# Kernel tuning notes

Hardware: AMD Instinct MI355X
Metric: run time of the kernel (lower is better)

The kernel has to match this reference:

```python
import jax, jax.numpy as jnp
import numpy as np


def _relative_position_index(ws):
    # matches SpatialAttention.build with qWh=qWw=kWh=kWw=ws
    coords = np.stack(np.meshgrid(np.arange(ws), np.arange(ws), indexing='ij'))
    cf = coords.reshape(2, -1)  # [2, N]
    rel = (cf[:, :, None] - cf[:, None, :]).transpose(1, 2, 0)  # [N, N, 2]
    rel[:, :, 0] += ws - 1
    rel[:, :, 1] += ws - 1
    rel[:, :, 0] *= 2 * ws - 1
    return rel.sum(-1)  # [N, N] int in [0, (2*ws-1)^2)


def _shift_mask(H, W, ws, ss):
    # standard Swin shifted-window attention mask: [num_windows, N, N]
    img = np.zeros((H, W))
    cnt = 0
    for h in (slice(0, -ws), slice(-ws, -ss), slice(-ss, None)):
        for w in (slice(0, -ws), slice(-ws, -ss), slice(-ss, None)):
            img[h, w] = cnt
            cnt += 1
    win = img.reshape(H // ws, ws, W // ws, ws).transpose(0, 2, 1, 3).reshape(-1, ws * ws)
    diff = win[:, None, :] - win[:, :, None]
    return np.where(diff != 0, -100.0, 0.0).astype(np.float32)


def _window_partition(x, ws):
    B, H, W, C = x.shape
    x = x.reshape(B, H // ws, ws, W // ws, ws, C)
    x = x.transpose(0, 1, 3, 2, 4, 5)
    return x.reshape(-1, ws, ws, C)  # [B*nW, ws, ws, C]


def _window_reverse(x, ws, H, W):
    C = x.shape[-1]
    x = x.reshape(-1, H // ws, W // ws, ws, ws, C)
    x = x.transpose(0, 1, 3, 2, 4, 5)
    return x.reshape(-1, H, W, C)


def setup_inputs() -> dict:
    key = jax.random.key(0)
    k1, k2, k3, k4 = jax.random.split(key, 4)
    B, H, W, C = 16, 64, 64, 512
    num_heads, ws = 16, 8
    return {
        'q': jax.random.normal(k1, (B, H, W, C), dtype=jnp.float32),
        'k': jax.random.normal(k2, (B, H, W, C), dtype=jnp.float32),
        'v': jax.random.normal(k3, (B, H, W, C), dtype=jnp.float32),
        'bias_table': jax.random.normal(k4, ((2 * ws - 1) ** 2, num_heads), dtype=jnp.float32) * 0.02,
        'num_heads': num_heads,
        'window_size': ws,
        'shift_size': 4,
    }


def reference(q, k, v, bias_table, num_heads, window_size, shift_size):
    B, H, W, C = q.shape
    ws, ss = window_size, shift_size
    N = ws * ws
    hd = C // num_heads
    scale = hd ** -0.5

    # cyclic shift
    q = jnp.roll(q, (-ss, -ss), axis=(1, 2))
    k = jnp.roll(k, (-ss, -ss), axis=(1, 2))
    v = jnp.roll(v, (-ss, -ss), axis=(1, 2))

    # window partition -> [B*nW, heads, N, hd]
    def to_heads(x):
        x = _window_partition(x, ws).reshape(-1, N, num_heads, hd)
        return x.transpose(0, 2, 1, 3)

    qh, kh, vh = to_heads(q), to_heads(k), to_heads(v)

    attn = jnp.einsum('bhid,bhjd->bhij', qh * scale, kh)  # [BnW, h, N, N]

    # gathered relative position bias: [1, h, N, N]
    idx = jnp.asarray(_relative_position_index(ws))
    rel_bias = bias_table[idx.reshape(-1)].reshape(N, N, num_heads).transpose(2, 0, 1)
    attn = attn + rel_bias[None]

    # shifted-window mask: [nW, N, N]
    mask = jnp.asarray(_shift_mask(H, W, ws, ss))
    nW = mask.shape[0]
    attn = attn.reshape(-1, nW, num_heads, N, N) + mask[None, :, None]
    attn = attn.reshape(-1, num_heads, N, N)

    attn = jax.nn.softmax(attn, axis=-1)

    x = jnp.einsum('bhij,bhjd->bihd', attn, vh).reshape(-1, ws, ws, C)
    x = _window_reverse(x, ws, H, W)
    x = jnp.roll(x, (ss, ss), axis=(1, 2))  # reverse cyclic shift
    return x
```

## Files before the change

### kernel.cpp

```cpp
#include <hip/hip_runtime.h>

#define TB 16
#define NHEADS 16
#define HD 32
#define WS 8
#define SS 4

typedef __attribute__((ext_vector_type(8))) __bf16 bf16x8;
typedef __attribute__((ext_vector_type(4))) float f32x4;

__device__ __forceinline__ unsigned short f2bf(float f) {
    unsigned u = __float_as_uint(f);
    u += 0x7fff + ((u >> 16) & 1);
    return (unsigned short)(u >> 16);
}
__device__ __forceinline__ unsigned pk2(float a, float b) {
    return (unsigned)f2bf(a) | ((unsigned)f2bf(b) << 16);
}
__device__ __forceinline__ float bf2f(unsigned short h) {
    return __uint_as_float(((unsigned)h) << 16);
}

#define OFF_Q 0
#define OFF_K 5120
#define OFF_P 0
#define OFF_V 10240
#define OFF_S 14848
#define OFF_B 23552

__global__ __launch_bounds__(64, 2)
void swin_attn_mfma(const float* __restrict__ q,
                    const float* __restrict__ k,
                    const float* __restrict__ v,
                    const float* __restrict__ bias_table,
                    float* __restrict__ out)
{
    __shared__ __align__(16) char smem[24464];
    char* sQ = smem + OFF_Q;
    char* sK = smem + OFF_K;
    char* sP = smem + OFF_P;
    char* sV = smem + OFF_V;
    char* sS = smem + OFF_S;
    float* sB = (float*)(smem + OFF_B);

    const int blk  = blockIdx.x;
    const int head = blk & (NHEADS - 1);
    const int win  = (blk >> 4) & 63;
    const int b    = blk >> 10;
    const int wh   = win >> 3;
    const int ww   = win & 7;

    const int lane = threadIdx.x;
    const int ih = lane >> 3, iw = lane & 7;
    const int quad = lane >> 4, lm = lane & 15;

    for (int t = lane; t < 225; t += 64)
        sB[t] = bias_table[t * NHEADS + head];

    const int gh = (wh * WS + ih + SS) & 63;
    const int gw = (ww * WS + iw + SS) & 63;
    const size_t rowbase = (((size_t)b * 64 + gh) * 64 + gw) * 512 + (size_t)head * HD;

    {
        const float scale = 0.17677669529663687f;
        const float4* qrow = (const float4*)(q + rowbase);
        uint4* qd = (uint4*)(sQ + lane * 80);
        #pragma unroll
        for (int t = 0; t < 4; ++t) {
            float4 a = qrow[2 * t], c = qrow[2 * t + 1];
            uint4 w;
            w.x = pk2(a.x * scale, a.y * scale);
            w.y = pk2(a.z * scale, a.w * scale);
            w.z = pk2(c.x * scale, c.y * scale);
            w.w = pk2(c.z * scale, c.w * scale);
            qd[t] = w;
        }
        const float4* krow = (const float4*)(k + rowbase);
        uint4* kd = (uint4*)(sK + lane * 80);
        #pragma unroll
        for (int t = 0; t < 4; ++t) {
            float4 a = krow[2 * t], c = krow[2 * t + 1];
            uint4 w;
            w.x = pk2(a.x, a.y);
            w.y = pk2(a.z, a.w);
            w.z = pk2(c.x, c.y);
            w.w = pk2(c.z, c.w);
            kd[t] = w;
        }
        const float4* vrow = (const float4*)(v + rowbase);
        #pragma unroll
        for (int t = 0; t < 8; ++t) {
            float4 x = vrow[t];
            *(unsigned short*)(sV + (4 * t + 0) * 144 + lane * 2) = f2bf(x.x);
            *(unsigned short*)(sV + (4 * t + 1) * 144 + lane * 2) = f2bf(x.y);
            *(unsigned short*)(sV + (4 * t + 2) * 144 + lane * 2) = f2bf(x.z);
            *(unsigned short*)(sV + (4 * t + 3) * 144 + lane * 2) = f2bf(x.w);
        }
    }
    __syncthreads();

    bf16x8 qa[4], kb[4];
    #pragma unroll
    for (int mt = 0; mt < 4; ++mt)
        qa[mt] = *(const bf16x8*)(sQ + (16 * mt + lm) * 80 + quad * 16);
    #pragma unroll
    for (int nt = 0; nt < 4; ++nt)
        kb[nt] = *(const bf16x8*)(sK + (16 * nt + lm) * 80 + quad * 16);

    f32x4 Sacc[4][4];
    #pragma unroll
    for (int mt = 0; mt < 4; ++mt)
        #pragma unroll
        for (int nt = 0; nt < 4; ++nt) {
            f32x4 z = {0.f, 0.f, 0.f, 0.f};
            Sacc[mt][nt] = __builtin_amdgcn_mfma_f32_16x16x32_bf16(qa[mt], kb[nt], z, 0, 0, 0);
        }

    #pragma unroll
    for (int mt = 0; mt < 4; ++mt)
        #pragma unroll
        for (int nt = 0; nt < 4; ++nt) {
            f32x4 s4 = Sacc[mt][nt];
            uint2 w;
            w.x = pk2(s4[0], s4[1]);
            w.y = pk2(s4[2], s4[3]);
            *(uint2*)(sS + (16 * nt + lm) * 136 + (16 * mt + 4 * quad) * 2) = w;
        }
    __syncthreads();

    float p[64];
    float l = 0.f;
    const bool eh = (wh == 7), ew = (ww == 7);
    const bool aH = (ih < 4), aW = (iw < 4);
    const char* bb = (const char*)sB + 4 * (ih * 15 + iw);
    const char* sc = sS + lane * 2;
    #pragma unroll
    for (int j = 0; j < 64; ++j) {
        const int jh = j >> 3, jw = j & 7;
        float s = bf2f(*(const unsigned short*)(sc + j * 136));
        s += *(const float*)(bb + 4 * ((7 - jh) * 15 + (7 - jw)));
        bool ok = (!eh || (aH == (jh < 4))) && (!ew || (aW == (jw < 4)));
        float e = ok ? __expf(s) : 0.f;
        p[j] = e;
        l += e;
    }
    const float rl = 1.f / l;
    {
        uint4* pd = (uint4*)(sP + lane * 144);
        #pragma unroll
        for (int t = 0; t < 8; ++t) {
            uint4 w;
            w.x = pk2(p[8 * t + 0] * rl, p[8 * t + 1] * rl);
            w.y = pk2(p[8 * t + 2] * rl, p[8 * t + 3] * rl);
            w.z = pk2(p[8 * t + 4] * rl, p[8 * t + 5] * rl);
            w.w = pk2(p[8 * t + 6] * rl, p[8 * t + 7] * rl);
            pd[t] = w;
        }
    }
    __syncthreads();

    bf16x8 pa[4][2], vb[2][2];
    #pragma unroll
    for (int mt = 0; mt < 4; ++mt)
        #pragma unroll
        for (int ks = 0; ks < 2; ++ks)
            pa[mt][ks] = *(const bf16x8*)(sP + (16 * mt + lm) * 144 + ks * 64 + quad * 16);
    #pragma unroll
    for (int nt = 0; nt < 2; ++nt)
        #pragma unroll
        for (int ks = 0; ks < 2; ++ks)
            vb[nt][ks] = *(const bf16x8*)(sV + (16 * nt + lm) * 144 + ks * 64 + quad * 16);

    f32x4 O[4][2];
    #pragma unroll
    for (int mt = 0; mt < 4; ++mt)
        #pragma unroll
        for (int nt = 0; nt < 2; ++nt) {
            f32x4 z = {0.f, 0.f, 0.f, 0.f};
            z = __builtin_amdgcn_mfma_f32_16x16x32_bf16(pa[mt][0], vb[nt][0], z, 0, 0, 0);
            O[mt][nt] = __builtin_amdgcn_mfma_f32_16x16x32_bf16(pa[mt][1], vb[nt][1], z, 0, 0, 0);
        }

    #pragma unroll
    for (int mt = 0; mt < 4; ++mt)
        #pragma unroll
        for (int r = 0; r < 4; ++r) {
            const int i = 16 * mt + 4 * quad + r;
            const int ghh = (wh * WS + (i >> 3) + SS) & 63;
            const int gww = (ww * WS + (i & 7) + SS) & 63;
            float* rp = out + (((size_t)b * 64 + ghh) * 64 + gww) * 512 + (size_t)head * HD + lm;
            rp[0]  = O[mt][0][r];
            rp[16] = O[mt][1][r];
        }
}

extern "C" void kernel_launch(void* const* d_in, const int* in_sizes, int n_in,
                              void* d_out, int out_size, void* d_ws, size_t ws_size,
                              hipStream_t stream) {
    const float* q  = (const float*)d_in[0];
    const float* k  = (const float*)d_in[1];
    const float* v  = (const float*)d_in[2];
    const float* bt = (const float*)d_in[3];
    float* out = (float*)d_out;

    dim3 grid(TB * 64 * NHEADS);
    dim3 block(64);
    swin_attn_mfma<<<grid, block, 0, stream>>>(q, k, v, bt, out);
}
```

Baseline: 438.9 us.

## Split window attention across four waves with in-register softmax

Each block now uses 256 threads (four waves). Wave 0 loads Q, wave 1 loads K, and waves 2 and 3 split V and the bias gather, so the global loads run in parallel. Each wave then computes one 16-row M tile of QK^T and applies bias, mask and exp directly on the MFMA accumulator registers. Row sums come from cross-lane shuffles, which removes the bf16 score round-trip through shared memory and the 64-element per-thread softmax loop. This lowers per-thread register and LDS pressure at the cost of an extra barrier and scattered 2-byte LDS stores for P.

```diff
diff --git a/kernel.cpp b/kernel.cpp
--- a/kernel.cpp
+++ b/kernel.cpp
@@ -17,30 +17,25 @@
 __device__ __forceinline__ unsigned pk2(float a, float b) {
     return (unsigned)f2bf(a) | ((unsigned)f2bf(b) << 16);
 }
-__device__ __forceinline__ float bf2f(unsigned short h) {
-    return __uint_as_float(((unsigned)h) << 16);
-}
 
 #define OFF_Q 0
 #define OFF_K 5120
 #define OFF_P 0
 #define OFF_V 10240
-#define OFF_S 14848
-#define OFF_B 23552
+#define OFF_B 14848
 
-__global__ __launch_bounds__(64, 2)
+__global__ __launch_bounds__(256, 8)
 void swin_attn_mfma(const float* __restrict__ q,
                     const float* __restrict__ k,
                     const float* __restrict__ v,
                     const float* __restrict__ bias_table,
                     float* __restrict__ out)
 {
-    __shared__ __align__(16) char smem[24464];
+    __shared__ __align__(16) char smem[15760];
     char* sQ = smem + OFF_Q;
     char* sK = smem + OFF_K;
     char* sP = smem + OFF_P;
     char* sV = smem + OFF_V;
-    char* sS = smem + OFF_S;
     float* sB = (float*)(smem + OFF_B);
 
     const int blk  = blockIdx.x;
@@ -50,148 +45,141 @@
     const int wh   = win >> 3;
     const int ww   = win & 7;
 
-    const int lane = threadIdx.x;
-    const int ih = lane >> 3, iw = lane & 7;
+    const int tid  = threadIdx.x;
+    const int wave = tid >> 6;
+    const int lane = tid & 63;
     const int quad = lane >> 4, lm = lane & 15;
 
-    for (int t = lane; t < 225; t += 64)
-        sB[t] = bias_table[t * NHEADS + head];
+    {
+        const int ih = lane >> 3, iw = lane & 7;
+        const int gh = (wh * WS + ih + SS) & 63;
+        const int gw = (ww * WS + iw + SS) & 63;
+        const size_t rowbase = (((size_t)b * 64 + gh) * 64 + gw) * 512 + (size_t)head * HD;
 
-    const int gh = (wh * WS + ih + SS) & 63;
-    const int gw = (ww * WS + iw + SS) & 63;
-    const size_t rowbase = (((size_t)b * 64 + gh) * 64 + gw) * 512 + (size_t)head * HD;
-
-    {
-        const float scale = 0.17677669529663687f;
-        const float4* qrow = (const float4*)(q + rowbase);
-        uint4* qd = (uint4*)(sQ + lane * 80);
-        #pragma unroll
-        for (int t = 0; t < 4; ++t) {
-            float4 a = qrow[2 * t], c = qrow[2 * t + 1];
-            uint4 w;
-            w.x = pk2(a.x * scale, a.y * scale);
-            w.y = pk2(a.z * scale, a.w * scale);
-            w.z = pk2(c.x * scale, c.y * scale);
-            w.w = pk2(c.z * scale, c.w * scale);
-            qd[t] = w;
-        }
-        const float4* krow = (const float4*)(k + rowbase);
-        uint4* kd = (uint4*)(sK + lane * 80);
-        #pragma unroll
-        for (int t = 0; t < 4; ++t) {
-            float4 a = krow[2 * t], c = krow[2 * t + 1];
-            uint4 w;
-            w.x = pk2(a.x, a.y);
-            w.y = pk2(a.z, a.w);
-            w.z = pk2(c.x, c.y);
-            w.w = pk2(c.z, c.w);
-            kd[t] = w;
-        }
-        const float4* vrow = (const float4*)(v + rowbase);
-        #pragma unroll
-        for (int t = 0; t < 8; ++t) {
-            float4 x = vrow[t];
-            *(unsigned short*)(sV + (4 * t + 0) * 144 + lane * 2) = f2bf(x.x);
-            *(unsigned short*)(sV + (4 * t + 1) * 144 + lane * 2) = f2bf(x.y);
-            *(unsigned short*)(sV + (4 * t + 2) * 144 + lane * 2) = f2bf(x.z);
-            *(unsigned short*)(sV + (4 * t + 3) * 144 + lane * 2) = f2bf(x.w);
+        if (wave == 0) {
+            const float scale = 0.17677669529663687f;
+            const float4* qrow = (const float4*)(q + rowbase);
+            uint4* qd = (uint4*)(sQ + lane * 80);
+            #pragma unroll
+            for (int t = 0; t < 4; ++t) {
+                float4 a = qrow[2 * t], c = qrow[2 * t + 1];
+                uint4 w;
+                w.x = pk2(a.x * scale, a.y * scale);
+                w.y = pk2(a.z * scale, a.w * scale);
+                w.z = pk2(c.x * scale, c.y * scale);
+                w.w = pk2(c.z * scale, c.w * scale);
+                qd[t] = w;
+            }
+        } else if (wave == 1) {
+            const float4* krow = (const float4*)(k + rowbase);
+            uint4* kd = (uint4*)(sK + lane * 80);
+            #pragma unroll
+            for (int t = 0; t < 4; ++t) {
+                float4 a = krow[2 * t], c = krow[2 * t + 1];
+                uint4 w;
+                w.x = pk2(a.x, a.y);
+                w.y = pk2(a.z, a.w);
+                w.z = pk2(c.x, c.y);
+                w.w = pk2(c.z, c.w);
+                kd[t] = w;
+            }
+        } else {
+            const int t0 = (wave == 2) ? 0 : 4;
+            const float4* vrow = (const float4*)(v + rowbase);
+            #pragma unroll
+            for (int t = 0; t < 4; ++t) {
+                float4 x = vrow[t0 + t];
+                const int ch = 4 * (t0 + t);
+                *(unsigned short*)(sV + (ch + 0) * 144 + lane * 2) = f2bf(x.x);
+                *(unsigned short*)(sV + (ch + 1) * 144 + lane * 2) = f2bf(x.y);
+                *(unsigned short*)(sV + (ch + 2) * 144 + lane * 2) = f2bf(x.z);
+                *(unsigned short*)(sV + (ch + 3) * 144 + lane * 2) = f2bf(x.w);
+            }
+            if (wave == 3) {
+                #pragma unroll
+                for (int t = lane; t < 225; t += 64)
+                    sB[t] = bias_table[t * NHEADS + head];
+            }
         }
     }
     __syncthreads();
 
-    bf16x8 qa[4], kb[4];
-    #pragma unroll
-    for (int mt = 0; mt < 4; ++mt)
-        qa[mt] = *(const bf16x8*)(sQ + (16 * mt + lm) * 80 + quad * 16);
+    bf16x8 qa = *(const bf16x8*)(sQ + (16 * wave + lm) * 80 + quad * 16);
+    bf16x8 kb[4];
     #pragma unroll
     for (int nt = 0; nt < 4; ++nt)
         kb[nt] = *(const bf16x8*)(sK + (16 * nt + lm) * 80 + quad * 16);
 
-    f32x4 Sacc[4][4];
+    f32x4 S[4];
     #pragma unroll
-    for (int mt = 0; mt < 4; ++mt)
+    for (int nt = 0; nt < 4; ++nt) {
+        f32x4 z = {0.f, 0.f, 0.f, 0.f};
+        S[nt] = __builtin_amdgcn_mfma_f32_16x16x32_bf16(qa, kb[nt], z, 0, 0, 0);
+    }
+
+    const bool eh = (wh == 7), ew = (ww == 7);
+    const int ihh = 2 * wave + (quad >> 1);
+    const int jw  = lm & 7;
+    float part[4] = {0.f, 0.f, 0.f, 0.f};
+    #pragma unroll
+    for (int nt = 0; nt < 4; ++nt) {
+        const int jh = 2 * nt + (lm >> 3);
+        const bool okh = !eh || ((ihh < 4) == (jh < 4));
         #pragma unroll
-        for (int nt = 0; nt < 4; ++nt) {
-            f32x4 z = {0.f, 0.f, 0.f, 0.f};
-            Sacc[mt][nt] = __builtin_amdgcn_mfma_f32_16x16x32_bf16(qa[mt], kb[nt], z, 0, 0, 0);
+        for (int r = 0; r < 4; ++r) {
+            const int iww = 4 * (quad & 1) + r;
+            float s = S[nt][r] + sB[(ihh - jh + 7) * 15 + (iww - jw + 7)];
+            bool ok = okh && (!ew || ((iww < 4) == (jw < 4)));
+            float e = ok ? __expf(s) : 0.f;
+            S[nt][r] = e;
+            part[r] += e;
         }
+    }
+    #pragma unroll
+    for (int m = 1; m <= 8; m <<= 1)
+        #pragma unroll
+        for (int r = 0; r < 4; ++r)
+            part[r] += __shfl_xor(part[r], m, 64);
+    float rl[4];
+    #pragma unroll
+    for (int r = 0; r < 4; ++r)
+        rl[r] = 1.f / part[r];
 
+    __syncthreads();
     #pragma unroll
-    for (int mt = 0; mt < 4; ++mt)
+    for (int nt = 0; nt < 4; ++nt)
         #pragma unroll
-        for (int nt = 0; nt < 4; ++nt) {
-            f32x4 s4 = Sacc[mt][nt];
-            uint2 w;
-            w.x = pk2(s4[0], s4[1]);
-            w.y = pk2(s4[2], s4[3]);
-            *(uint2*)(sS + (16 * nt + lm) * 136 + (16 * mt + 4 * quad) * 2) = w;
-        }
+        for (int r = 0; r < 4; ++r)
+            *(unsigned short*)(sP + (16 * wave + 4 * quad + r) * 144 + (16 * nt + lm) * 2)
+                = f2bf(S[nt][r] * rl[r]);
     __syncthreads();
 
-    float p[64];
-    float l = 0.f;
-    const bool eh = (wh == 7), ew = (ww == 7);
-    const bool aH = (ih < 4), aW = (iw < 4);
-    const char* bb = (const char*)sB + 4 * (ih * 15 + iw);
-    const char* sc = sS + lane * 2;
-    #pragma unroll
-    for (int j = 0; j < 64; ++j) {
-        const int jh = j >> 3, jw = j & 7;
-        float s = bf2f(*(const unsigned short*)(sc + j * 136));
-        s += *(const float*)(bb + 4 * ((7 - jh) * 15 + (7 - jw)));
-        bool ok = (!eh || (aH == (jh < 4))) && (!ew || (aW == (jw < 4)));
-        float e = ok ? __expf(s) : 0.f;
-        p[j] = e;
-        l += e;
-    }
-    const float rl = 1.f / l;
-    {
-        uint4* pd = (uint4*)(sP + lane * 144);
-        #pragma unroll
-        for (int t = 0; t < 8; ++t) {
-            uint4 w;
-            w.x = pk2(p[8 * t + 0] * rl, p[8 * t + 1] * rl);
-            w.y = pk2(p[8 * t + 2] * rl, p[8 * t + 3] * rl);
-            w.z = pk2(p[8 * t + 4] * rl, p[8 * t + 5] * rl);
-            w.w = pk2(p[8 * t + 6] * rl, p[8 * t + 7] * rl);
-            pd[t] = w;
-        }
-    }
-    __syncthreads();
-
-    bf16x8 pa[4][2], vb[2][2];
-    #pragma unroll
-    for (int mt = 0; mt < 4; ++mt)
-        #pragma unroll
-        for (int ks = 0; ks < 2; ++ks)
-            pa[mt][ks] = *(const bf16x8*)(sP + (16 * mt + lm) * 144 + ks * 64 + quad * 16);
+    bf16x8 pa0 = *(const bf16x8*)(sP + (16 * wave + lm) * 144 + quad * 16);
+    bf16x8 pa1 = *(const bf16x8*)(sP + (16 * wave + lm) * 144 + 64 + quad * 16);
+    bf16x8 vb[2][2];
     #pragma unroll
     for (int nt = 0; nt < 2; ++nt)
         #pragma unroll
         for (int ks = 0; ks < 2; ++ks)
             vb[nt][ks] = *(const bf16x8*)(sV + (16 * nt + lm) * 144 + ks * 64 + quad * 16);
 
-    f32x4 O[4][2];
+    f32x4 O[2];
     #pragma unroll
-    for (int mt = 0; mt < 4; ++mt)
-        #pragma unroll
-        for (int nt = 0; nt < 2; ++nt) {
-            f32x4 z = {0.f, 0.f, 0.f, 0.f};
-            z = __builtin_amdgcn_mfma_f32_16x16x32_bf16(pa[mt][0], vb[nt][0], z, 0, 0, 0);
-            O[mt][nt] = __builtin_amdgcn_mfma_f32_16x16x32_bf16(pa[mt][1], vb[nt][1], z, 0, 0, 0);
-        }
+    for (int nt = 0; nt < 2; ++nt) {
+        f32x4 z = {0.f, 0.f, 0.f, 0.f};
+        z = __builtin_amdgcn_mfma_f32_16x16x32_bf16(pa0, vb[nt][0], z, 0, 0, 0);
+        O[nt] = __builtin_amdgcn_mfma_f32_16x16x32_bf16(pa1, vb[nt][1], z, 0, 0, 0);
+    }
 
     #pragma unroll
-    for (int mt = 0; mt < 4; ++mt)
-        #pragma unroll
-        for (int r = 0; r < 4; ++r) {
-            const int i = 16 * mt + 4 * quad + r;
-            const int ghh = (wh * WS + (i >> 3) + SS) & 63;
-            const int gww = (ww * WS + (i & 7) + SS) & 63;
-            float* rp = out + (((size_t)b * 64 + ghh) * 64 + gww) * 512 + (size_t)head * HD + lm;
-            rp[0]  = O[mt][0][r];
-            rp[16] = O[mt][1][r];
-        }
+    for (int r = 0; r < 4; ++r) {
+        const int i = 16 * wave + 4 * quad + r;
+        const int ghh = (wh * WS + (i >> 3) + SS) & 63;
+        const int gww = (ww * WS + (i & 7) + SS) & 63;
+        float* rp = out + (((size_t)b * 64 + ghh) * 64 + gww) * 512 + (size_t)head * HD + lm;
+        rp[0]  = O[0][r];
+        rp[16] = O[1][r];
+    }
 }
 
 extern "C" void kernel_launch(void* const* d_in, const int* in_sizes, int n_in,
@@ -204,6 +192,6 @@
     float* out = (float*)d_out;
 
     dim3 grid(TB * 64 * NHEADS);
-    dim3 block(64);
+    dim3 block(256);
     swin_attn_mfma<<<grid, block, 0, stream>>>(q, k, v, bt, out);
 }
```

Result: no change. 431.0 us (-1.8%).
